# Optimization experiments

Hardware: AMD Instinct MI355X
Metric: run time of the kernel (lower is better)

The kernel has to match this reference:

```python
import jax, jax.numpy as jnp
import numpy as np

B, T, I, H, C = 128, 1024, 256, 512, 10


def setup_inputs() -> dict:
    key = jax.random.key(0)
    ks = jax.random.split(key, 11)
    s = 0.05
    return {
        "x": jax.random.normal(ks[0], (B, T, I), dtype=jnp.float32),
        "W_ih1": jax.random.normal(ks[1], (4 * H, I), dtype=jnp.float32) * s,
        "W_hh1": jax.random.normal(ks[2], (4 * H, H), dtype=jnp.float32) * s,
        "b_ih1": jax.random.normal(ks[3], (4 * H,), dtype=jnp.float32) * s,
        "b_hh1": jax.random.normal(ks[4], (4 * H,), dtype=jnp.float32) * s,
        "W_ih2": jax.random.normal(ks[5], (4 * H, H), dtype=jnp.float32) * s,
        "W_hh2": jax.random.normal(ks[6], (4 * H, H), dtype=jnp.float32) * s,
        "b_ih2": jax.random.normal(ks[7], (4 * H,), dtype=jnp.float32) * s,
        "b_hh2": jax.random.normal(ks[8], (4 * H,), dtype=jnp.float32) * s,
        "W_out": jax.random.normal(ks[9], (C, H), dtype=jnp.float32) * s,
        "b_out": jax.random.normal(ks[10], (C,), dtype=jnp.float32) * s,
    }


def _lstm_cell(x_t, h, c, W_ih, W_hh, b_ih, b_hh):
    # PyTorch LSTMCell: gates ordered (i, f, g, o), each of size H
    gates = x_t @ W_ih.T + b_ih + h @ W_hh.T + b_hh  # [B, 4H]
    i, f, g, o = jnp.split(gates, 4, axis=-1)
    i = jax.nn.sigmoid(i)
    f = jax.nn.sigmoid(f)
    g = jnp.tanh(g)
    o = jax.nn.sigmoid(o)
    c_new = f * c + i * g
    h_new = o * jnp.tanh(c_new)
    return h_new, c_new


def reference(x, W_ih1, W_hh1, b_ih1, b_hh1, W_ih2, W_hh2, b_ih2, b_hh2, W_out, b_out):
    Bv = x.shape[0]
    Hv = W_hh1.shape[1]
    zeros = jnp.zeros((Bv, Hv), dtype=x.dtype)
    init = (zeros, zeros, zeros, zeros)  # h1, c1, h2, c2

    def step(carry, x_t):
        h1, c1, h2, c2 = carry
        h1, c1 = _lstm_cell(x_t, h1, c1, W_ih1, W_hh1, b_ih1, b_hh1)
        h2, c2 = _lstm_cell(h1, h2, c2, W_ih2, W_hh2, b_ih2, b_hh2)
        return (h1, c1, h2, c2), None

    xs = jnp.swapaxes(x, 0, 1)  # [T, B, I]
    (h1, c1, h2, c2), _ = jax.lax.scan(step, init, xs)
    return h2 @ W_out.T + b_out  # [B, C]
```

## Files before the change

kernel.cpp:

```cpp
#include <hip/hip_runtime.h>
#include <hip/hip_bf16.h>
#include <hip/hip_cooperative_groups.h>

namespace cg = cooperative_groups;

#define B_ 128
#define TT 1024
#define I_ 256
#define H_ 512
#define BH (B_*H_)

typedef __bf16 bf16x8 __attribute__((ext_vector_type(8)));
typedef float  f32x4  __attribute__((ext_vector_type(4)));
typedef unsigned int u32;

__device__ __forceinline__ float sigm(float x){ return 1.f/(1.f+__expf(-x)); }
__device__ __forceinline__ float tanh_(float x){
    float t=__expf(-2.f*fabsf(x)); float r=(1.f-t)/(1.f+t); return copysignf(r,x);
}
__device__ __forceinline__ unsigned bf16bits(float f){
    unsigned x=__float_as_uint(f);
    return (x + 0x7fffu + ((x>>16)&1u)) >> 16;
}


__global__ void pack_w1(const float* __restrict__ Wih, const float* __restrict__ Whh,
                        const float* __restrict__ bih, const float* __restrict__ bhh,
                        __hip_bfloat16* __restrict__ Wp, float* __restrict__ bcp) {
    int idx = blockIdx.x*256 + threadIdx.x;
    int low = idx & 511;
    int e = low & 7, row = (low>>3)&15, ksub = low>>7;
    int rest = idx >> 9;
    int ks = rest % 24, pbt = rest / 24;
    int p = pbt*16 + row;
    int g = p & 3, j = p >> 2;
    int wrow = g*512 + j;
    int k = ks*32 + ksub*8 + e;
    float v = (k < 256) ? Wih[wrow*256 + k] : Whh[(size_t)wrow*512 + (k-256)];
    Wp[idx] = __float2bfloat16(v);
    if (ks==0 && ksub==0 && e==0) bcp[p] = bih[wrow] + bhh[wrow];
}

__global__ void pack_w2(const float* __restrict__ Wih, const float* __restrict__ Whh,
                        const float* __restrict__ bih, const float* __restrict__ bhh,
                        __hip_bfloat16* __restrict__ Wp, float* __restrict__ bcp) {
    int idx = blockIdx.x*256 + threadIdx.x;
    int low = idx & 511;
    int e = low & 7, row = (low>>3)&15, ksub = low>>7;
    int rest = idx >> 9;
    int ks = rest & 31, pbt = rest >> 5;
    int p = pbt*16 + row;
    int g = p & 3, j = p >> 2;
    int wrow = g*512 + j;
    int k = ks*32 + ksub*8 + e;
    float v = (k < 512) ? Wih[(size_t)wrow*512 + k] : Whh[(size_t)wrow*512 + (k-512)];
    Wp[idx] = __float2bfloat16(v);
    if (ks==0 && ksub==0 && e==0) bcp[p] = bih[wrow] + bhh[wrow];
}

__global__ void xconv(const float* __restrict__ x, __hip_bfloat16* __restrict__ xbT) {
    long idx = (long)blockIdx.x * 256 + threadIdx.x;
    long base = idx * 4;
    int i = (int)(base & (I_ - 1));
    int t = (int)((base >> 8) & (TT - 1));
    int b = (int)(base >> 18);
    const float4 v = *(const float4*)(x + ((long)b * TT + t) * I_ + i);
    __hip_bfloat16* o = xbT + ((long)t * B_ + b) * I_ + i;
    o[0] = __float2bfloat16(v.x); o[1] = __float2bfloat16(v.y);
    o[2] = __float2bfloat16(v.z); o[3] = __float2bfloat16(v.w);
}

__device__ __forceinline__ void epi_store(const f32x4& acc, const f32x4& bias, float& c,
                                          int jg, int bg, __hip_bfloat16* hout) {
    float iv = sigm(acc[0] + bias[0]);
    float fv = sigm(acc[1] + bias[1]);
    float gv = tanh_(acc[2] + bias[2]);
    float ov = sigm(acc[3] + bias[3]);
    c = fv*c + iv*gv;
    float hv = ov * tanh_(c);
    unsigned hb = bf16bits(hv);
    unsigned pr = (unsigned)__shfl_xor((int)hb, 16);
    if ((jg & 1) == 0) {
        u32 val = hb | (pr << 16);
        __hip_atomic_store((u32*)(hout + (size_t)bg*H_ + jg), val,
                           __ATOMIC_RELAXED, __HIP_MEMORY_SCOPE_AGENT);
    }
}


__global__ void __launch_bounds__(256, 1) lstm_coop(
    const __hip_bfloat16* __restrict__ xbT,
    const __hip_bfloat16* __restrict__ W1p, const __hip_bfloat16* __restrict__ W2p,
    const float* __restrict__ bcp1, const float* __restrict__ bcp2,
    __hip_bfloat16* __restrict__ h1b, __hip_bfloat16* __restrict__ h2b)
{
    const int bid = blockIdx.x, tid = threadIdx.x;
    const int lane = tid & 63, w = tid >> 6;
    const int layer = bid >> 7;
    const int r = bid & 127;
    const int pt = r >> 2, bt = r & 3;
    const int q = lane >> 4, col = lane & 15;
    const int bhalf = w >> 1, ppair = w & 1;
    const int bg = bt*32 + bhalf*16 + col;
    const int jg0 = pt*16 + ppair*8 + q;
    const int jg1 = jg0 + 4;
    cg::grid_group g = cg::this_grid();

    if (layer == 0) {
        bf16x8 wr[48];
        const bf16x8* Wg = reinterpret_cast<const bf16x8*>(W1p);
#pragma unroll
        for (int a = 0; a < 2; ++a) {
            int pbt = pt*4 + ppair*2 + a;
#pragma unroll
            for (int ks = 0; ks < 24; ++ks)
                wr[a*24 + ks] = Wg[(pbt*24 + ks)*64 + q*16 + col];
        }
        const f32x4 bias0 = *reinterpret_cast<const f32x4*>(bcp1 + jg0*4);
        const f32x4 bias1 = *reinterpret_cast<const f32x4*>(bcp1 + jg1*4);
        float c0 = 0.f, c1 = 0.f;
        bf16x8 xc[8];
        {
            const __hip_bfloat16* xr = xbT + (size_t)bg*I_ + q*8;
#pragma unroll
            for (int s = 0; s < 8; ++s) xc[s] = *reinterpret_cast<const bf16x8*>(xr + s*32);
        }

        for (int p = 0; p <= TT; ++p) {
            if (p < TT) {
                const __hip_bfloat16* h1r = h1b + ((p-1)&1)*BH + (size_t)bg*H_ + q*8;
                f32x4 acc0 = {0.f,0.f,0.f,0.f}, acc1 = {0.f,0.f,0.f,0.f};
#pragma unroll
                for (int s = 0; s < 8; ++s) {
                    acc0 = __builtin_amdgcn_mfma_f32_16x16x32_bf16(wr[s],    xc[s], acc0, 0,0,0);
                    acc1 = __builtin_amdgcn_mfma_f32_16x16x32_bf16(wr[24+s], xc[s], acc1, 0,0,0);
                }
#pragma unroll
                for (int kc = 0; kc < 2; ++kc) {
                    bf16x8 bfr[8];
#pragma unroll
                    for (int s = 0; s < 8; ++s)
                        bfr[s] = *reinterpret_cast<const bf16x8*>(h1r + (kc*8+s)*32);
#pragma unroll
                    for (int s = 0; s < 8; ++s) {
                        acc0 = __builtin_amdgcn_mfma_f32_16x16x32_bf16(wr[8+kc*8+s],  bfr[s], acc0, 0,0,0);
                        acc1 = __builtin_amdgcn_mfma_f32_16x16x32_bf16(wr[32+kc*8+s], bfr[s], acc1, 0,0,0);
                    }
                }
                if (p + 1 < TT) {
                    const __hip_bfloat16* xr2 = xbT + ((size_t)(p+1)*B_ + bg)*I_ + q*8;
#pragma unroll
                    for (int s = 0; s < 8; ++s) xc[s] = *reinterpret_cast<const bf16x8*>(xr2 + s*32);
                }
                __hip_bfloat16* hout = h1b + (p&1)*BH;
                epi_store(acc0, bias0, c0, jg0, bg, hout);
                epi_store(acc1, bias1, c1, jg1, bg, hout);
            }
            g.sync();
        }
    } else {
        bf16x8 wr[64];
        const bf16x8* Wg = reinterpret_cast<const bf16x8*>(W2p);
#pragma unroll
        for (int a = 0; a < 2; ++a) {
            int pbt = pt*4 + ppair*2 + a;
#pragma unroll
            for (int ks = 0; ks < 32; ++ks)
                wr[a*32 + ks] = Wg[(pbt*32 + ks)*64 + q*16 + col];
        }
        const f32x4 bias0 = *reinterpret_cast<const f32x4*>(bcp2 + jg0*4);
        const f32x4 bias1 = *reinterpret_cast<const f32x4*>(bcp2 + jg1*4);
        float c0 = 0.f, c1 = 0.f;

        for (int p = 0; p <= TT; ++p) {
            if (p >= 1) {
                const __hip_bfloat16* h1r = h1b + ((p-1)&1)*BH + (size_t)bg*H_ + q*8;
                const __hip_bfloat16* h2r = h2b + (p&1)*BH     + (size_t)bg*H_ + q*8;
                f32x4 acc0 = {0.f,0.f,0.f,0.f}, acc1 = {0.f,0.f,0.f,0.f};
#pragma unroll
                for (int kc = 0; kc < 2; ++kc) {
                    bf16x8 bfr[8];
#pragma unroll
                    for (int s = 0; s < 8; ++s)
                        bfr[s] = *reinterpret_cast<const bf16x8*>(h1r + (kc*8+s)*32);
#pragma unroll
                    for (int s = 0; s < 8; ++s) {
                        acc0 = __builtin_amdgcn_mfma_f32_16x16x32_bf16(wr[kc*8+s],    bfr[s], acc0, 0,0,0);
                        acc1 = __builtin_amdgcn_mfma_f32_16x16x32_bf16(wr[32+kc*8+s], bfr[s], acc1, 0,0,0);
                    }
                }
#pragma unroll
                for (int kc = 0; kc < 2; ++kc) {
                    bf16x8 bfr[8];
#pragma unroll
                    for (int s = 0; s < 8; ++s)
                        bfr[s] = *reinterpret_cast<const bf16x8*>(h2r + (kc*8+s)*32);
#pragma unroll
                    for (int s = 0; s < 8; ++s) {
                        acc0 = __builtin_amdgcn_mfma_f32_16x16x32_bf16(wr[16+kc*8+s], bfr[s], acc0, 0,0,0);
                        acc1 = __builtin_amdgcn_mfma_f32_16x16x32_bf16(wr[48+kc*8+s], bfr[s], acc1, 0,0,0);
                    }
                }
                __hip_bfloat16* hout = h2b + ((p-1)&1)*BH;
                epi_store(acc0, bias0, c0, jg0, bg, hout);
                epi_store(acc1, bias1, c1, jg1, bg, hout);
            }
            g.sync();
        }
    }
}

__global__ void __launch_bounds__(256, 1) lstm_step(
    int p,
    const __hip_bfloat16* __restrict__ xbT,
    const __hip_bfloat16* __restrict__ W1p, const __hip_bfloat16* __restrict__ W2p,
    const float* __restrict__ bcp1, const float* __restrict__ bcp2,
    __hip_bfloat16* __restrict__ h1b, __hip_bfloat16* __restrict__ h2b,
    float* __restrict__ cw1, float* __restrict__ cw2)
{
    const int bid = blockIdx.x, tid = threadIdx.x;
    const int lane = tid & 63, w = tid >> 6;
    const int layer = bid >> 7;
    const int r = bid & 127;
    const int pt = r >> 2, bt = r & 3;
    const int q = lane >> 4, col = lane & 15;
    const int bhalf = w >> 1, ppair = w & 1;
    const int bg = bt*32 + bhalf*16 + col;
    const int jg0 = pt*16 + ppair*8 + q;
    const int jg1 = jg0 + 4;

    if (layer == 0) {
        if (p >= TT) return;
        bf16x8 wr[48];
        const bf16x8* Wg = reinterpret_cast<const bf16x8*>(W1p);
#pragma unroll
        for (int a = 0; a < 2; ++a) {
            int pbt = pt*4 + ppair*2 + a;
#pragma unroll
            for (int ks = 0; ks < 24; ++ks)
                wr[a*24 + ks] = Wg[(pbt*24 + ks)*64 + q*16 + col];
        }
        const f32x4 bias0 = *reinterpret_cast<const f32x4*>(bcp1 + jg0*4);
        const f32x4 bias1 = *reinterpret_cast<const f32x4*>(bcp1 + jg1*4);
        float c0 = cw1[(size_t)bg*H_ + jg0];
        float c1 = cw1[(size_t)bg*H_ + jg1];
        const __hip_bfloat16* xr = xbT + ((size_t)p*B_ + bg)*I_ + q*8;
        const __hip_bfloat16* h1r = h1b + ((p-1)&1)*BH + (size_t)bg*H_ + q*8;
        f32x4 acc0 = {0.f,0.f,0.f,0.f}, acc1 = {0.f,0.f,0.f,0.f};
#pragma unroll
        for (int s = 0; s < 8; ++s) {
            bf16x8 xv = *reinterpret_cast<const bf16x8*>(xr + s*32);
            acc0 = __builtin_amdgcn_mfma_f32_16x16x32_bf16(wr[s],    xv, acc0, 0,0,0);
            acc1 = __builtin_amdgcn_mfma_f32_16x16x32_bf16(wr[24+s], xv, acc1, 0,0,0);
        }
#pragma unroll
        for (int kc = 0; kc < 2; ++kc) {
#pragma unroll
            for (int s = 0; s < 8; ++s) {
                bf16x8 bv = *reinterpret_cast<const bf16x8*>(h1r + (kc*8+s)*32);
                acc0 = __builtin_amdgcn_mfma_f32_16x16x32_bf16(wr[8+kc*8+s],  bv, acc0, 0,0,0);
                acc1 = __builtin_amdgcn_mfma_f32_16x16x32_bf16(wr[32+kc*8+s], bv, acc1, 0,0,0);
            }
        }
        __hip_bfloat16* hout = h1b + (p&1)*BH;
        epi_store(acc0, bias0, c0, jg0, bg, hout);
        epi_store(acc1, bias1, c1, jg1, bg, hout);
        cw1[(size_t)bg*H_ + jg0] = c0;
        cw1[(size_t)bg*H_ + jg1] = c1;
    } else {
        if (p < 1) return;
        bf16x8 wr[64];
        const bf16x8* Wg = reinterpret_cast<const bf16x8*>(W2p);
#pragma unroll
        for (int a = 0; a < 2; ++a) {
            int pbt = pt*4 + ppair*2 + a;
#pragma unroll
            for (int ks = 0; ks < 32; ++ks)
                wr[a*32 + ks] = Wg[(pbt*32 + ks)*64 + q*16 + col];
        }
        const f32x4 bias0 = *reinterpret_cast<const f32x4*>(bcp2 + jg0*4);
        const f32x4 bias1 = *reinterpret_cast<const f32x4*>(bcp2 + jg1*4);
        float c0 = cw2[(size_t)bg*H_ + jg0];
        float c1 = cw2[(size_t)bg*H_ + jg1];
        const __hip_bfloat16* h1r = h1b + ((p-1)&1)*BH + (size_t)bg*H_ + q*8;
        const __hip_bfloat16* h2r = h2b + (p&1)*BH     + (size_t)bg*H_ + q*8;
        f32x4 acc0 = {0.f,0.f,0.f,0.f}, acc1 = {0.f,0.f,0.f,0.f};
#pragma unroll
        for (int kc = 0; kc < 2; ++kc) {
#pragma unroll
            for (int s = 0; s < 8; ++s) {
                bf16x8 bv = *reinterpret_cast<const bf16x8*>(h1r + (kc*8+s)*32);
                acc0 = __builtin_amdgcn_mfma_f32_16x16x32_bf16(wr[kc*8+s],    bv, acc0, 0,0,0);
                acc1 = __builtin_amdgcn_mfma_f32_16x16x32_bf16(wr[32+kc*8+s], bv, acc1, 0,0,0);
            }
        }
#pragma unroll
        for (int kc = 0; kc < 2; ++kc) {
#pragma unroll
            for (int s = 0; s < 8; ++s) {
                bf16x8 bv = *reinterpret_cast<const bf16x8*>(h2r + (kc*8+s)*32);
                acc0 = __builtin_amdgcn_mfma_f32_16x16x32_bf16(wr[16+kc*8+s], bv, acc0, 0,0,0);
                acc1 = __builtin_amdgcn_mfma_f32_16x16x32_bf16(wr[48+kc*8+s], bv, acc1, 0,0,0);
            }
        }
        __hip_bfloat16* hout = h2b + ((p-1)&1)*BH;
        epi_store(acc0, bias0, c0, jg0, bg, hout);
        epi_store(acc1, bias1, c1, jg1, bg, hout);
        cw2[(size_t)bg*H_ + jg0] = c0;
        cw2[(size_t)bg*H_ + jg1] = c1;
    }
}

__global__ void proj_kernel(const __hip_bfloat16* __restrict__ h2,
                            const float* __restrict__ Wout, const float* __restrict__ bout,
                            float* __restrict__ out) {
    int b = blockIdx.x, lane = threadIdx.x;
    const bf16x8 h8 = *reinterpret_cast<const bf16x8*>(h2 + b * 512 + lane * 8);
    float hv[8];
#pragma unroll
    for (int e = 0; e < 8; ++e) hv[e] = (float)h8[e];
    for (int c = 0; c < 10; ++c) {
        const float4 w0 = *(const float4*)(Wout + c * 512 + lane * 8);
        const float4 w1 = *(const float4*)(Wout + c * 512 + lane * 8 + 4);
        float s = hv[0] * w0.x + hv[1] * w0.y + hv[2] * w0.z + hv[3] * w0.w +
                  hv[4] * w1.x + hv[5] * w1.y + hv[6] * w1.z + hv[7] * w1.w;
#pragma unroll
        for (int off = 32; off > 0; off >>= 1) s += __shfl_down(s, off);
        if (lane == 0) out[b * 10 + c] = s + bout[c];
    }
}

extern "C" void kernel_launch(void* const* d_in, const int* in_sizes, int n_in,
                              void* d_out, int out_size, void* d_ws, size_t ws_size,
                              hipStream_t stream) {
    const float* x    = (const float*)d_in[0];
    const float* Wih1 = (const float*)d_in[1];
    const float* Whh1 = (const float*)d_in[2];
    const float* bih1 = (const float*)d_in[3];
    const float* bhh1 = (const float*)d_in[4];
    const float* Wih2 = (const float*)d_in[5];
    const float* Whh2 = (const float*)d_in[6];
    const float* bih2 = (const float*)d_in[7];
    const float* bhh2 = (const float*)d_in[8];
    const float* Wout = (const float*)d_in[9];
    const float* bout = (const float*)d_in[10];
    float* out = (float*)d_out;

    char* ws = (char*)d_ws;
    size_t off = 0;
    auto alloc = [&](size_t bytes) -> void* {
        void* pp = ws + off;
        off += (bytes + 255) & ~(size_t)255;
        return pp;
    };
    __hip_bfloat16* W1p = (__hip_bfloat16*)alloc((size_t)128*24*512*2);
    __hip_bfloat16* W2p = (__hip_bfloat16*)alloc((size_t)128*32*512*2);
    float* bcp1 = (float*)alloc(2048*4);
    float* bcp2 = (float*)alloc(2048*4);
    __hip_bfloat16* h1b = (__hip_bfloat16*)alloc((size_t)2*BH*2);
    __hip_bfloat16* h2b = (__hip_bfloat16*)alloc((size_t)2*BH*2);
    float* cw1 = (float*)alloc((size_t)BH*4);
    float* cw2 = (float*)alloc((size_t)BH*4);
    __hip_bfloat16* xbT = (__hip_bfloat16*)alloc((size_t)TT*B_*I_*2);
    if (off > ws_size) return;

    hipMemsetAsync(h1b, 0, (size_t)4*BH*2 + (size_t)2*BH*4, stream);

    pack_w1<<<(128*24*512)/256, 256, 0, stream>>>(Wih1, Whh1, bih1, bhh1, W1p, bcp1);
    pack_w2<<<(128*32*512)/256, 256, 0, stream>>>(Wih2, Whh2, bih2, bhh2, W2p, bcp2);
    xconv<<<((long)TT*B_*I_/4)/256, 256, 0, stream>>>(x, xbT);

    int dev = 0;
    hipGetDevice(&dev);
    int nCU = 0;
    hipDeviceGetAttribute(&nCU, hipDeviceAttributeMultiprocessorCount, dev);
    int perCU = 0;
    hipOccupancyMaxActiveBlocksPerMultiprocessor(&perCU, lstm_coop, 256, 0);

    const __hip_bfloat16* xbT_ = xbT;
    const __hip_bfloat16* W1p_ = W1p;
    const __hip_bfloat16* W2p_ = W2p;
    const float* bcp1_ = bcp1;
    const float* bcp2_ = bcp2;
    __hip_bfloat16* h1b_ = h1b;
    __hip_bfloat16* h2b_ = h2b;

    if ((long)perCU * nCU >= 256) {
        void* args[] = {&xbT_, &W1p_, &W2p_, &bcp1_, &bcp2_, &h1b_, &h2b_};
        hipLaunchCooperativeKernel((void*)lstm_coop, dim3(256), dim3(256), args, 0, stream);
    } else {
        for (int p = 0; p <= TT; ++p)
            lstm_step<<<256, 256, 0, stream>>>(p, xbT, W1p, W2p, bcp1, bcp2,
                                               h1b, h2b, cw1, cw2);
    }

    proj_kernel<<<B_, 64, 0, stream>>>(h2b + BH, Wout, bout, out);
}
```

Baseline: 9.409 ms.

## Replace grid-wide sync with per-batch-tile flag polling and triple buffering

Removes the cooperative grid.sync between timesteps. Each block now publishes a per-tile progress flag and polls only the 32 producer flags of its batch tile, so layers and batch tiles can run skewed and pipeline. Hidden-state buffers become triple-buffered so producers can run a step ahead without overwriting data still being read. Blocks double to 512 threads, so each wave handles one gate group instead of two, which lowers register pressure and raises MFMA parallelism. The cost is system-scope atomics, explicit cache writeback and invalidate instructions, and spin-polling overhead.

```diff
diff --git a/kernel.cpp b/kernel.cpp
--- a/kernel.cpp
+++ b/kernel.cpp
@@ -1,8 +1,5 @@
 #include <hip/hip_runtime.h>
 #include <hip/hip_bf16.h>
-#include <hip/hip_cooperative_groups.h>
-
-namespace cg = cooperative_groups;
 
 #define B_ 128
 #define TT 1024
@@ -71,7 +68,7 @@
 }
 
 __device__ __forceinline__ void epi_store(const f32x4& acc, const f32x4& bias, float& c,
-                                          int jg, int bg, __hip_bfloat16* hout) {
+                                          int jg, int bg, __hip_bfloat16* base) {
     float iv = sigm(acc[0] + bias[0]);
     float fv = sigm(acc[1] + bias[1]);
     float gv = tanh_(acc[2] + bias[2]);
@@ -82,17 +79,20 @@
     unsigned pr = (unsigned)__shfl_xor((int)hb, 16);
     if ((jg & 1) == 0) {
         u32 val = hb | (pr << 16);
-        __hip_atomic_store((u32*)(hout + (size_t)bg*H_ + jg), val,
-                           __ATOMIC_RELAXED, __HIP_MEMORY_SCOPE_AGENT);
+        __hip_atomic_store((u32*)(base + (size_t)bg*H_ + jg), val,
+                           __ATOMIC_RELAXED, __HIP_MEMORY_SCOPE_SYSTEM);
     }
 }
 
-
-__global__ void __launch_bounds__(256, 1) lstm_coop(
+#define MFMA(A,Bv,C) __builtin_amdgcn_mfma_f32_16x16x32_bf16((A),(Bv),(C),0,0,0)
+
+
+__global__ void __launch_bounds__(512, 2) lstm_coop(
     const __hip_bfloat16* __restrict__ xbT,
     const __hip_bfloat16* __restrict__ W1p, const __hip_bfloat16* __restrict__ W2p,
     const float* __restrict__ bcp1, const float* __restrict__ bcp2,
-    __hip_bfloat16* __restrict__ h1b, __hip_bfloat16* __restrict__ h2b)
+    __hip_bfloat16* __restrict__ h1b, __hip_bfloat16* __restrict__ h2b,
+    int* __restrict__ flags)
 {
     const int bid = blockIdx.x, tid = threadIdx.x;
     const int lane = tid & 63, w = tid >> 6;
@@ -100,25 +100,44 @@
     const int r = bid & 127;
     const int pt = r >> 2, bt = r & 3;
     const int q = lane >> 4, col = lane & 15;
-    const int bhalf = w >> 1, ppair = w & 1;
+    const int bhalf = w >> 2, ppair = w & 3;
     const int bg = bt*32 + bhalf*16 + col;
-    const int jg0 = pt*16 + ppair*8 + q;
-    const int jg1 = jg0 + 4;
-    cg::grid_group g = cg::this_grid();
+    const int jg = pt*16 + ppair*4 + q;
+    const int pbt = pt*4 + ppair;
+    int* fl = flags + bt*1024;
+    int* myflag = fl + (layer*32 + pt)*16;
+    const size_t rdoff = (size_t)bg*H_ + q*8;
+
+    auto pollwait = [&](int tA, int tB){
+        if (tid < 64) {
+            const int t = (lane < 32) ? tA : tB;
+            const int* fp = fl + lane*16;
+            while (__ballot(__hip_atomic_load(fp, __ATOMIC_RELAXED,
+                                              __HIP_MEMORY_SCOPE_SYSTEM) < t)) {}
+            asm volatile("buffer_inv sc0 sc1" ::: "memory");
+        }
+        __syncthreads();
+    };
+    auto post = [&](int val){
+        __syncthreads();
+        if (tid == 0) {
+            asm volatile("buffer_wbl2 sc0 sc1\n\ts_waitcnt vmcnt(0)" ::: "memory");
+            __hip_atomic_store(myflag, val, __ATOMIC_RELAXED, __HIP_MEMORY_SCOPE_SYSTEM);
+        }
+    };
 
     if (layer == 0) {
-        bf16x8 wr[48];
+        bf16x8 wr[24];
         const bf16x8* Wg = reinterpret_cast<const bf16x8*>(W1p);
 #pragma unroll
-        for (int a = 0; a < 2; ++a) {
-            int pbt = pt*4 + ppair*2 + a;
-#pragma unroll
-            for (int ks = 0; ks < 24; ++ks)
-                wr[a*24 + ks] = Wg[(pbt*24 + ks)*64 + q*16 + col];
-        }
-        const f32x4 bias0 = *reinterpret_cast<const f32x4*>(bcp1 + jg0*4);
-        const f32x4 bias1 = *reinterpret_cast<const f32x4*>(bcp1 + jg1*4);
-        float c0 = 0.f, c1 = 0.f;
+        for (int ks = 0; ks < 24; ++ks)
+            wr[ks] = Wg[(pbt*24 + ks)*64 + q*16 + col];
+        const f32x4 bias = *reinterpret_cast<const f32x4*>(bcp1 + jg*4);
+        float c0 = 0.f;
+        __hip_bfloat16* pb0 = h1b;
+        __hip_bfloat16* pb1 = h1b + BH;
+        __hip_bfloat16* pb2 = h1b + 2*BH;
+
         bf16x8 xc[8];
         {
             const __hip_bfloat16* xr = xbT + (size_t)bg*I_ + q*8;
@@ -126,86 +145,71 @@
             for (int s = 0; s < 8; ++s) xc[s] = *reinterpret_cast<const bf16x8*>(xr + s*32);
         }
 
-        for (int p = 0; p <= TT; ++p) {
-            if (p < TT) {
-                const __hip_bfloat16* h1r = h1b + ((p-1)&1)*BH + (size_t)bg*H_ + q*8;
-                f32x4 acc0 = {0.f,0.f,0.f,0.f}, acc1 = {0.f,0.f,0.f,0.f};
-#pragma unroll
-                for (int s = 0; s < 8; ++s) {
-                    acc0 = __builtin_amdgcn_mfma_f32_16x16x32_bf16(wr[s],    xc[s], acc0, 0,0,0);
-                    acc1 = __builtin_amdgcn_mfma_f32_16x16x32_bf16(wr[24+s], xc[s], acc1, 0,0,0);
-                }
-#pragma unroll
-                for (int kc = 0; kc < 2; ++kc) {
-                    bf16x8 bfr[8];
-#pragma unroll
-                    for (int s = 0; s < 8; ++s)
-                        bfr[s] = *reinterpret_cast<const bf16x8*>(h1r + (kc*8+s)*32);
-#pragma unroll
-                    for (int s = 0; s < 8; ++s) {
-                        acc0 = __builtin_amdgcn_mfma_f32_16x16x32_bf16(wr[8+kc*8+s],  bfr[s], acc0, 0,0,0);
-                        acc1 = __builtin_amdgcn_mfma_f32_16x16x32_bf16(wr[32+kc*8+s], bfr[s], acc1, 0,0,0);
-                    }
-                }
-                if (p + 1 < TT) {
-                    const __hip_bfloat16* xr2 = xbT + ((size_t)(p+1)*B_ + bg)*I_ + q*8;
-#pragma unroll
-                    for (int s = 0; s < 8; ++s) xc[s] = *reinterpret_cast<const bf16x8*>(xr2 + s*32);
-                }
-                __hip_bfloat16* hout = h1b + (p&1)*BH;
-                epi_store(acc0, bias0, c0, jg0, bg, hout);
-                epi_store(acc1, bias1, c1, jg1, bg, hout);
+        for (int p = 0; p < TT; ++p) {
+            pollwait(p, p-1);
+            const __hip_bfloat16* rd = pb2 + rdoff;
+            bf16x8 fA[8], fB[8];
+#pragma unroll
+            for (int s = 0; s < 8; ++s) fA[s] = *reinterpret_cast<const bf16x8*>(rd + s*32);
+#pragma unroll
+            for (int s = 0; s < 8; ++s) fB[s] = *reinterpret_cast<const bf16x8*>(rd + (8+s)*32);
+            f32x4 acc = {0.f,0.f,0.f,0.f};
+#pragma unroll
+            for (int s = 0; s < 8; ++s) acc = MFMA(wr[s],    xc[s], acc);
+#pragma unroll
+            for (int s = 0; s < 8; ++s) acc = MFMA(wr[8+s],  fA[s], acc);
+#pragma unroll
+            for (int s = 0; s < 8; ++s) acc = MFMA(wr[16+s], fB[s], acc);
+            epi_store(acc, bias, c0, jg, bg, pb0);
+            post(p+1);
+            if (p + 1 < TT) {
+                const __hip_bfloat16* xr = xbT + ((size_t)(p+1)*B_ + bg)*I_ + q*8;
+#pragma unroll
+                for (int s = 0; s < 8; ++s) xc[s] = *reinterpret_cast<const bf16x8*>(xr + s*32);
             }
-            g.sync();
+            __hip_bfloat16* t0 = pb0; pb0 = pb1; pb1 = pb2; pb2 = t0;
         }
     } else {
-        bf16x8 wr[64];
+        bf16x8 wr[32];
         const bf16x8* Wg = reinterpret_cast<const bf16x8*>(W2p);
 #pragma unroll
-        for (int a = 0; a < 2; ++a) {
-            int pbt = pt*4 + ppair*2 + a;
-#pragma unroll
-            for (int ks = 0; ks < 32; ++ks)
-                wr[a*32 + ks] = Wg[(pbt*32 + ks)*64 + q*16 + col];
-        }
-        const f32x4 bias0 = *reinterpret_cast<const f32x4*>(bcp2 + jg0*4);
-        const f32x4 bias1 = *reinterpret_cast<const f32x4*>(bcp2 + jg1*4);
-        float c0 = 0.f, c1 = 0.f;
-
-        for (int p = 0; p <= TT; ++p) {
-            if (p >= 1) {
-                const __hip_bfloat16* h1r = h1b + ((p-1)&1)*BH + (size_t)bg*H_ + q*8;
-                const __hip_bfloat16* h2r = h2b + (p&1)*BH     + (size_t)bg*H_ + q*8;
-                f32x4 acc0 = {0.f,0.f,0.f,0.f}, acc1 = {0.f,0.f,0.f,0.f};
-#pragma unroll
-                for (int kc = 0; kc < 2; ++kc) {
-                    bf16x8 bfr[8];
-#pragma unroll
-                    for (int s = 0; s < 8; ++s)
-                        bfr[s] = *reinterpret_cast<const bf16x8*>(h1r + (kc*8+s)*32);
-#pragma unroll
-                    for (int s = 0; s < 8; ++s) {
-                        acc0 = __builtin_amdgcn_mfma_f32_16x16x32_bf16(wr[kc*8+s],    bfr[s], acc0, 0,0,0);
-                        acc1 = __builtin_amdgcn_mfma_f32_16x16x32_bf16(wr[32+kc*8+s], bfr[s], acc1, 0,0,0);
-                    }
-                }
-#pragma unroll
-                for (int kc = 0; kc < 2; ++kc) {
-                    bf16x8 bfr[8];
-#pragma unroll
-                    for (int s = 0; s < 8; ++s)
-                        bfr[s] = *reinterpret_cast<const bf16x8*>(h2r + (kc*8+s)*32);
-#pragma unroll
-                    for (int s = 0; s < 8; ++s) {
-                        acc0 = __builtin_amdgcn_mfma_f32_16x16x32_bf16(wr[16+kc*8+s], bfr[s], acc0, 0,0,0);
-                        acc1 = __builtin_amdgcn_mfma_f32_16x16x32_bf16(wr[48+kc*8+s], bfr[s], acc1, 0,0,0);
-                    }
-                }
-                __hip_bfloat16* hout = h2b + ((p-1)&1)*BH;
-                epi_store(acc0, bias0, c0, jg0, bg, hout);
-                epi_store(acc1, bias1, c1, jg1, bg, hout);
-            }
-            g.sync();
+        for (int ks = 0; ks < 32; ++ks)
+            wr[ks] = Wg[(pbt*32 + ks)*64 + q*16 + col];
+        const f32x4 bias = *reinterpret_cast<const f32x4*>(bcp2 + jg*4);
+        float c0 = 0.f;
+        __hip_bfloat16* g0 = h1b + BH;
+        __hip_bfloat16* g1 = h1b + 2*BH;
+        __hip_bfloat16* g2 = h1b;
+        __hip_bfloat16* v0 = h2b + BH;
+        __hip_bfloat16* v1 = h2b + 2*BH;
+        __hip_bfloat16* v2 = h2b;
+
+        for (int p = 1; p <= TT; ++p) {
+            pollwait(p, p);
+            const __hip_bfloat16* rd1 = g2 + rdoff;
+            const __hip_bfloat16* rd2 = v1 + rdoff;
+            bf16x8 fA[8], fB[8];
+#pragma unroll
+            for (int s = 0; s < 8; ++s) fA[s] = *reinterpret_cast<const bf16x8*>(rd1 + s*32);
+#pragma unroll
+            for (int s = 0; s < 8; ++s) fB[s] = *reinterpret_cast<const bf16x8*>(rd1 + (8+s)*32);
+            f32x4 acc = {0.f,0.f,0.f,0.f};
+#pragma unroll
+            for (int s = 0; s < 8; ++s) acc = MFMA(wr[s], fA[s], acc);
+#pragma unroll
+            for (int s = 0; s < 8; ++s) fA[s] = *reinterpret_cast<const bf16x8*>(rd2 + s*32);
+#pragma unroll
+            for (int s = 0; s < 8; ++s) acc = MFMA(wr[8+s], fB[s], acc);
+#pragma unroll
+            for (int s = 0; s < 8; ++s) fB[s] = *reinterpret_cast<const bf16x8*>(rd2 + (8+s)*32);
+#pragma unroll
+            for (int s = 0; s < 8; ++s) acc = MFMA(wr[16+s], fA[s], acc);
+#pragma unroll
+            for (int s = 0; s < 8; ++s) acc = MFMA(wr[24+s], fB[s], acc);
+            epi_store(acc, bias, c0, jg, bg, v2);
+            post(p+1);
+            __hip_bfloat16* t0 = g0; g0 = g1; g1 = g2; g2 = t0;
+            __hip_bfloat16* t1 = v0; v0 = v1; v1 = v2; v2 = t1;
         }
     }
 }
@@ -250,16 +254,16 @@
 #pragma unroll
         for (int s = 0; s < 8; ++s) {
             bf16x8 xv = *reinterpret_cast<const bf16x8*>(xr + s*32);
-            acc0 = __builtin_amdgcn_mfma_f32_16x16x32_bf16(wr[s],    xv, acc0, 0,0,0);
-            acc1 = __builtin_amdgcn_mfma_f32_16x16x32_bf16(wr[24+s], xv, acc1, 0,0,0);
+            acc0 = MFMA(wr[s],    xv, acc0);
+            acc1 = MFMA(wr[24+s], xv, acc1);
         }
 #pragma unroll
         for (int kc = 0; kc < 2; ++kc) {
 #pragma unroll
             for (int s = 0; s < 8; ++s) {
                 bf16x8 bv = *reinterpret_cast<const bf16x8*>(h1r + (kc*8+s)*32);
-                acc0 = __builtin_amdgcn_mfma_f32_16x16x32_bf16(wr[8+kc*8+s],  bv, acc0, 0,0,0);
-                acc1 = __builtin_amdgcn_mfma_f32_16x16x32_bf16(wr[32+kc*8+s], bv, acc1, 0,0,0);
+                acc0 = MFMA(wr[8+kc*8+s],  bv, acc0);
+                acc1 = MFMA(wr[32+kc*8+s], bv, acc1);
             }
         }
         __hip_bfloat16* hout = h1b + (p&1)*BH;
@@ -290,8 +294,8 @@
 #pragma unroll
             for (int s = 0; s < 8; ++s) {
                 bf16x8 bv = *reinterpret_cast<const bf16x8*>(h1r + (kc*8+s)*32);
-                acc0 = __builtin_amdgcn_mfma_f32_16x16x32_bf16(wr[kc*8+s],    bv, acc0, 0,0,0);
-                acc1 = __builtin_amdgcn_mfma_f32_16x16x32_bf16(wr[32+kc*8+s], bv, acc1, 0,0,0);
+                acc0 = MFMA(wr[kc*8+s],    bv, acc0);
+                acc1 = MFMA(wr[32+kc*8+s], bv, acc1);
             }
         }
 #pragma unroll
@@ -299,8 +303,8 @@
 #pragma unroll
             for (int s = 0; s < 8; ++s) {
                 bf16x8 bv = *reinterpret_cast<const bf16x8*>(h2r + (kc*8+s)*32);
-                acc0 = __builtin_amdgcn_mfma_f32_16x16x32_bf16(wr[16+kc*8+s], bv, acc0, 0,0,0);
-                acc1 = __builtin_amdgcn_mfma_f32_16x16x32_bf16(wr[48+kc*8+s], bv, acc1, 0,0,0);
+                acc0 = MFMA(wr[16+kc*8+s], bv, acc0);
+                acc1 = MFMA(wr[48+kc*8+s], bv, acc1);
             }
         }
         __hip_bfloat16* hout = h2b + ((p-1)&1)*BH;
@@ -357,14 +361,15 @@
     __hip_bfloat16* W2p = (__hip_bfloat16*)alloc((size_t)128*32*512*2);
     float* bcp1 = (float*)alloc(2048*4);
     float* bcp2 = (float*)alloc(2048*4);
-    __hip_bfloat16* h1b = (__hip_bfloat16*)alloc((size_t)2*BH*2);
-    __hip_bfloat16* h2b = (__hip_bfloat16*)alloc((size_t)2*BH*2);
+    __hip_bfloat16* h1b = (__hip_bfloat16*)alloc((size_t)3*BH*2);
+    __hip_bfloat16* h2b = (__hip_bfloat16*)alloc((size_t)3*BH*2);
     float* cw1 = (float*)alloc((size_t)BH*4);
     float* cw2 = (float*)alloc((size_t)BH*4);
+    int* flags = (int*)alloc(4096*4);
     __hip_bfloat16* xbT = (__hip_bfloat16*)alloc((size_t)TT*B_*I_*2);
     if (off > ws_size) return;
 
-    hipMemsetAsync(h1b, 0, (size_t)4*BH*2 + (size_t)2*BH*4, stream);
+    hipMemsetAsync(h1b, 0, (size_t)6*BH*2 + (size_t)2*BH*4 + 4096*4, stream);
 
     pack_w1<<<(128*24*512)/256, 256, 0, stream>>>(Wih1, Whh1, bih1, bhh1, W1p, bcp1);
     pack_w2<<<(128*32*512)/256, 256, 0, stream>>>(Wih2, Whh2, bih2, bhh2, W2p, bcp2);
@@ -375,7 +380,8 @@
     int nCU = 0;
     hipDeviceGetAttribute(&nCU, hipDeviceAttributeMultiprocessorCount, dev);
     int perCU = 0;
-    hipOccupancyMaxActiveBlocksPerMultiprocessor(&perCU, lstm_coop, 256, 0);
+    hipOccupancyMaxActiveBlocksPerMultiprocessor(&perCU, lstm_coop, 512, 0);
+    const bool useCoop = ((long)perCU * nCU >= 256);
 
     const __hip_bfloat16* xbT_ = xbT;
     const __hip_bfloat16* W1p_ = W1p;
@@ -384,15 +390,16 @@
     const float* bcp2_ = bcp2;
     __hip_bfloat16* h1b_ = h1b;
     __hip_bfloat16* h2b_ = h2b;
-
-    if ((long)perCU * nCU >= 256) {
-        void* args[] = {&xbT_, &W1p_, &W2p_, &bcp1_, &bcp2_, &h1b_, &h2b_};
-        hipLaunchCooperativeKernel((void*)lstm_coop, dim3(256), dim3(256), args, 0, stream);
+    int* flags_ = flags;
+
+    if (useCoop) {
+        void* args[] = {&xbT_, &W1p_, &W2p_, &bcp1_, &bcp2_, &h1b_, &h2b_, &flags_};
+        hipLaunchCooperativeKernel((void*)lstm_coop, dim3(256), dim3(512), args, 0, stream);
+        proj_kernel<<<B_, 64, 0, stream>>>(h2b, Wout, bout, out);
     } else {
         for (int p = 0; p <= TT; ++p)
             lstm_step<<<256, 256, 0, stream>>>(p, xbT, W1p, W2p, bcp1, bcp2,
                                                h1b, h2b, cw1, cw2);
+        proj_kernel<<<B_, 64, 0, stream>>>(h2b + BH, Wout, bout, out);
     }
-
-    proj_kernel<<<B_, 64, 0, stream>>>(h2b + BH, Wout, bout, out);
-}
+}
```

After: 9.321 ms. About the same (-0.9%).
